# Optimization experiments

Measured on AMD Instinct MI355X. Metric: run time of the kernel, lower is better.

## Reference

```python
import jax, jax.numpy as jnp
import numpy as np

NUM_NODE = 64   # number of FPS nodes
NSAMPLE = 64    # ball-query / knn group size
RADIUS = 0.3    # first ball-query radius
K_INTERP = 3    # knn for upsample interpolation
BN_EPS = 1e-5


def sqdist(a, b):
    # a [B,S,3], b [B,N,3] -> squared distances [B,S,N]
    return (jnp.sum(a * a, -1)[:, :, None] + jnp.sum(b * b, -1)[:, None, :]
            - 2.0 * jnp.einsum('bsc,bnc->bsn', a, b))


def index_points(points, idx):
    # points [B,C,N] or [B,C,N,1]; idx [B,...] -> gathered [B,C,...]
    if points.ndim == 4:
        points = points[..., 0]
    return jax.vmap(lambda p, i: p[:, i])(points, idx)


def farthest_point_sample(xyz, npoint):
    # xyz [B,3,N] -> idx [B,npoint]; deterministic start at index 0
    B, C, N = xyz.shape

    def body(carry, _):
        dist, far = carry
        centroid = jnp.take_along_axis(xyz, far[:, None, None], axis=2)  # [B,3,1]
        d = jnp.sum((xyz - centroid) ** 2, axis=1)                       # [B,N]
        dist = jnp.minimum(dist, d)
        nxt = jnp.argmax(dist, axis=-1)
        return (dist, nxt), far

    init = (jnp.full((B, N), 1e10, xyz.dtype), jnp.zeros((B,), jnp.int32))
    _, idxs = jax.lax.scan(body, init, None, length=npoint)
    return idxs.T  # [B,npoint]


def query_ball_point(radius, nsample, xyz, new_xyz):
    # xyz [B,3,N], new_xyz [B,3,S] -> group idx [B,S,nsample]
    N = xyz.shape[2]
    sqr = sqdist(jnp.transpose(new_xyz, (0, 2, 1)), jnp.transpose(xyz, (0, 2, 1)))  # [B,S,N]
    if radius is not None:
        idx = jnp.broadcast_to(jnp.arange(N, dtype=jnp.int32), sqr.shape)
        idx = jnp.where(sqr > radius * radius, N, idx)
        idx = jnp.sort(idx, axis=-1)[:, :, :nsample]
        first = idx[:, :, :1]
        idx = jnp.where(idx == N, first, idx)  # pad misses with first hit
    else:
        idx = jnp.argsort(sqr, axis=-1)[:, :, :nsample].astype(jnp.int32)  # knn
    return idx


def _forward(input_fea, input_loc, pred_w, res_w, res_b, bn_gamma, bn_beta):
    # input_fea [B,C,N,1], input_loc [B,3,N]
    fidx = farthest_point_sample(input_loc, NUM_NODE)        # [B,S]
    fpoint_loc = index_points(input_loc, fidx)               # [B,3,S]
    fpoint_fea = index_points(input_fea, fidx)               # [B,C,S]

    gidx = query_ball_point(RADIUS, NSAMPLE, input_loc, fpoint_loc)  # [B,S,K]
    group_fea = index_points(input_fea, gidx) - fpoint_fea[..., None]  # [B,C,S,K]

    # pred_offset: 1x1 conv (no bias) + tanh
    seman = jnp.tanh(jnp.einsum('oc,bcsk->bosk', pred_w, group_fea))  # [B,3,S,K]

    group_loc = index_points(input_loc, gidx) - fpoint_loc[..., None]  # [B,3,S,K]
    node_offset = jnp.mean(seman * group_loc, axis=-1)       # [B,3,S]
    node_loc = fpoint_loc + node_offset                      # [B,3,S]

    gidx2 = query_ball_point(None, NSAMPLE, input_loc, node_loc)  # knn, [B,S,K]

    # residual branch: 1x1 conv + BatchNorm (training-mode batch stats) + ReLU
    res = jnp.einsum('oc,bcnk->bonk', res_w, input_fea) + res_b[None, :, None, None]
    mean = jnp.mean(res, axis=(0, 2, 3), keepdims=True)
    var = jnp.var(res, axis=(0, 2, 3), keepdims=True)
    res = (res - mean) * jax.lax.rsqrt(var + BN_EPS)
    res = jax.nn.relu(res * bn_gamma[None, :, None, None] + bn_beta[None, :, None, None])

    group_res = index_points(res, gidx2)                     # [B,F,S,K]
    node_fea = jnp.max(group_res, axis=-1, keepdims=True)    # [B,F,S,1]

    # upsample_inter: inverse-distance weighted 3-NN interpolation back to N points
    d = sqdist(jnp.transpose(input_loc, (0, 2, 1)), jnp.transpose(node_loc, (0, 2, 1)))  # [B,N,S]
    neg_d, kidx = jax.lax.top_k(-d, K_INTERP)                # k smallest dists
    dists = jnp.maximum(-neg_d, 1e-10)                       # [B,N,k]
    w = 1.0 / dists
    w = w / jnp.sum(w, axis=-1, keepdims=True)               # [B,N,k]
    interp = jnp.sum(index_points(node_fea, kidx) * w[:, None], axis=-1)  # [B,F,N]

    output_fea = jnp.concatenate([input_fea[..., 0], interp], axis=1)[..., None]  # [B,C+F,N,1]
    return output_fea, node_fea, node_offset


def setup_inputs() -> dict:
    key = jax.random.key(0)
    k1, k2, k3, k4, k5 = jax.random.split(key, 5)
    B, C, N = 32, 64, 8192
    FC = 64
    input_fea = jax.random.normal(k1, (B, C, N, 1), dtype=jnp.float32)
    input_loc = jax.random.uniform(k2, (B, 3, N), dtype=jnp.float32)
    pred_w = jax.random.normal(k3, (3, C), dtype=jnp.float32) * (1.0 / np.sqrt(C))
    res_w = jax.random.normal(k4, (FC, C), dtype=jnp.float32) * (1.0 / np.sqrt(C))
    res_b = jnp.zeros((FC,), dtype=jnp.float32)
    bn_gamma = jnp.ones((FC,), dtype=jnp.float32)
    bn_beta = jnp.zeros((FC,), dtype=jnp.float32)
    return {"input_fea": input_fea, "input_loc": input_loc, "pred_w": pred_w,
            "res_w": res_w, "res_b": res_b, "bn_gamma": bn_gamma, "bn_beta": bn_beta}


def reference(input_fea, input_loc, pred_w, res_w, res_b, bn_gamma, bn_beta):
    return _forward(input_fea, input_loc, pred_w, res_w, res_b, bn_gamma, bn_beta)
```

## Files before the change

kernel.cpp:

```cpp
#include <hip/hip_runtime.h>
#include <math.h>

#define BB 32
#define NN 8192
#define CC 64
#define SS 64
#define KK 64

#define WS_FIDX   0
#define WS_NLOC   270336
#define WS_GIDX2  276480
#define WS_PART   407552
#define WS_TOT    2537472
#define WS_SCALE  2541632
#define WS_SHIFT  2541696


__device__ __forceinline__ void fps_body(int b, const float* __restrict__ loc,
                                         int* __restrict__ fidx,
                                         float (*wrv)[8], int (*wri)[8],
                                         float (*wrx)[8], float (*wry)[8],
                                         float (*wrz)[8]) {
#pragma clang fp contract(off)
  __builtin_amdgcn_s_setprio(1);
  int t = threadIdx.x;
  const float* lb = loc + (size_t)b * 3 * NN;
  float px[16], py[16], pz[16], dist[16];
#pragma unroll
  for (int k = 0; k < 16; k++) {
    int p = t + 512 * k;
    px[k] = lb[p];
    py[k] = lb[NN + p];
    pz[k] = lb[2 * NN + p];
    dist[k] = 1e10f;
  }
  int lane = t & 63, w = t >> 6;
  int far = 0;
  float cx = lb[0], cy = lb[NN], cz = lb[2 * NN];
  for (int it = 0; it < 64; it++) {
    if (t == 0) fidx[b * 64 + it] = far;
    float bv = -1.0f; int bi = 0;
    float bx = 0.f, by = 0.f, bz = 0.f;
#pragma unroll
    for (int k = 0; k < 16; k++) {
      float dx = px[k] - cx, dy = py[k] - cy, dz = pz[k] - cz;
      float d = (dx * dx + dy * dy) + dz * dz;
      float dm = dist[k];
      dm = d < dm ? d : dm;
      dist[k] = dm;
      if (dm > bv) { bv = dm; bi = t + 512 * k; bx = px[k]; by = py[k]; bz = pz[k]; }
    }
    float v = bv; int vi = bi;
    float vx = bx, vy = by, vz = bz;
#pragma unroll
    for (int off = 1; off < 64; off <<= 1) {
      float v2 = __shfl_xor(v, off, 64);
      int   i2 = __shfl_xor(vi, off, 64);
      float x2 = __shfl_xor(vx, off, 64);
      float y2 = __shfl_xor(vy, off, 64);
      float z2 = __shfl_xor(vz, off, 64);
      if (v2 > v || (v2 == v && i2 < vi)) { v = v2; vi = i2; vx = x2; vy = y2; vz = z2; }
    }
    int par = it & 1;
    if (lane == 0) {
      wrv[par][w] = v; wri[par][w] = vi;
      wrx[par][w] = vx; wry[par][w] = vy; wrz[par][w] = vz;
    }
    __syncthreads();
    float gv = wrv[par][0]; int gi = wri[par][0];
    float gx = wrx[par][0], gy = wry[par][0], gz = wrz[par][0];
#pragma unroll
    for (int w2 = 1; w2 < 8; w2++) {
      float v2 = wrv[par][w2]; int i2 = wri[par][w2];
      if (v2 > gv || (v2 == gv && i2 < gi)) {
        gv = v2; gi = i2;
        gx = wrx[par][w2]; gy = wry[par][w2]; gz = wrz[par][w2];
      }
    }
    far = gi;
    cx = gx; cy = gy; cz = gz;
  }
}

__device__ __forceinline__ void transpose_body(int tb, const float* __restrict__ fea,
                                               float* __restrict__ feaT, float* tile) {
  int b = tb >> 7;
  int n0 = (tb & 127) * 64;
  int t = threadIdx.x;
  const float* fb = fea + (size_t)b * (CC * NN);
#pragma unroll
  for (int m = 0; m < 8; m++) {
    int idx = m * 512 + t;
    int c = idx >> 6, nl = idx & 63;
    tile[c * 65 + nl] = fb[(size_t)c * NN + n0 + nl];
  }
  __syncthreads();
  float* ob = feaT + ((size_t)b * NN + n0) * 64;
#pragma unroll
  for (int m = 0; m < 8; m++) {
    int idx = m * 512 + t;
    int nl = idx >> 6, c = idx & 63;
    ob[idx] = tile[c * 65 + nl];
  }
}

__device__ __forceinline__ void cov_body(int cb, const float* __restrict__ fea,
                                         float* __restrict__ part,
                                         float* Sf, float* red) {
  int t = threadIdx.x, w = t >> 6, lane = t & 63;
  int i = lane >> 3, j = lane & 7;
  float acc[8][8];
  float rs[8];
#pragma unroll
  for (int r = 0; r < 8; r++) {
    rs[r] = 0.f;
#pragma unroll
    for (int r2 = 0; r2 < 8; r2++) acc[r][r2] = 0.f;
  }
  for (int q = 0; q < 4; q++) {
    int chunk = cb * 4 + q;
    int p0 = chunk * 128;
    int b = p0 >> 13, n0 = p0 & 8191;
    __syncthreads();
    const float* fb = fea + (size_t)b * (CC * NN) + n0;
    for (int m = 0; m < 16; m++) {
      int idx = m * 512 + t;
      int c = idx >> 7, pt = idx & 127;
      Sf[c * 133 + pt] = fb[(size_t)c * NN + pt];
    }
    __syncthreads();
    if (w < 4) {
      for (int pt = w * 32; pt < w * 32 + 32; pt++) {
        float a[8], bv[8];
#pragma unroll
        for (int r = 0; r < 8; r++) {
          a[r] = Sf[(8 * i + r) * 133 + pt];
          bv[r] = Sf[(8 * j + r) * 133 + pt];
        }
#pragma unroll
        for (int r = 0; r < 8; r++) {
          rs[r] += a[r];
#pragma unroll
          for (int r2 = 0; r2 < 8; r2++) acc[r][r2] = fmaf(a[r], bv[r2], acc[r][r2]);
        }
      }
    }
  }
  for (int ww = 0; ww < 4; ww++) {
    if (w == ww) {
#pragma unroll
      for (int r = 0; r < 8; r++) {
#pragma unroll
        for (int r2 = 0; r2 < 8; r2++) {
          int idx = (8 * i + r) * 64 + 8 * j + r2;
          if (ww == 0) red[idx] = acc[r][r2]; else red[idx] += acc[r][r2];
        }
        if (j == 0) {
          int ridx = 4096 + 8 * i + r;
          if (ww == 0) red[ridx] = rs[r]; else red[ridx] += rs[r];
        }
      }
    }
    __syncthreads();
  }
  float* pb = part + (size_t)cb * 4160;
  for (int idx = t; idx < 4160; idx += 512) pb[idx] = red[idx];
}

__global__ __launch_bounds__(512, 1) void phase1_kernel(const float* __restrict__ fea,
                                                        const float* __restrict__ loc,
                                                        float* __restrict__ feaT,
                                                        int* __restrict__ fidx,
                                                        float* __restrict__ part) {
  __shared__ __align__(16) char smem[50688];
  __shared__ float wrv[2][8], wrx[2][8], wry[2][8], wrz[2][8];
  __shared__ int wri[2][8];
  int blk = blockIdx.x;
  if (blk < 32) {
    fps_body(blk, loc, fidx, wrv, wri, wrx, wry, wrz);
  } else if (blk < 4128) {
    transpose_body(blk - 32, fea, feaT, (float*)smem);
  } else {
    cov_body(blk - 4128, fea, part, (float*)smem, (float*)(smem + 34048));
  }
}

__global__ __launch_bounds__(256) void mega_kernel(const float* __restrict__ loc,
                                                   const float* __restrict__ feaT,
                                                   const float* __restrict__ pw,
                                                   const int* __restrict__ fidx,
                                                   const float* __restrict__ part,
                                                   float* __restrict__ tot,
                                                   int* __restrict__ gidx2,
                                                   float* __restrict__ out_noff,
                                                   float* __restrict__ nloc) {
#pragma clang fp contract(off)
  int blk = blockIdx.x;
  if (blk >= 2048) {
    int e = (blk - 2048) * 256 + threadIdx.x;
    if (e < 4160) {
      float sum = 0.f;
      for (int b2 = 0; b2 < 512; b2++) sum += part[(size_t)b2 * 4160 + e];
      tot[e] = sum;
    }
    return;
  }
  int bs = blk, b = bs >> 6, s = bs & 63, t = threadIdx.x;
  int lane = t & 63, w = t >> 6;
  __shared__ unsigned keys[NN];
  __shared__ unsigned hist[4096];
  __shared__ unsigned partl[256];
  __shared__ float sf[64];
  __shared__ float spw[192];
  __shared__ float sl[3];
  __shared__ float sA[3];
  __shared__ int gidxL[64];
  __shared__ int sP, sC0, nOut, nCand;
  const float* lb = loc + (size_t)b * 3 * NN;

  if (t < 192) spw[t] = pw[t];
  if (w == 0) {
    int g = fidx[bs];
    sf[lane] = feaT[((size_t)b * NN + g) * 64 + lane];
    if (lane < 3) sl[lane] = lb[(size_t)lane * NN + g];
  }
  __syncthreads();

  if (w == 0) {
    float ax = sl[0], ay = sl[1], az = sl[2];
    float A = (ax * ax + ay * ay) + az * az;
    int count = 0, firsth = -1;
    for (int ch = 0; ch < 128 && count < 64; ch++) {
      int p = ch * 64 + lane;
      float bx = lb[p], by = lb[NN + p], bz = lb[2 * NN + p];
      float Bn = (bx * bx + by * by) + bz * bz;
      float dot = fmaf(az, bz, fmaf(ay, by, ax * bx));
      float sqr = (A + Bn) - 2.0f * dot;
      bool hit = !(sqr > 0.09f);
      unsigned long long m = __ballot(hit);
      if (m) {
        if (firsth < 0) firsth = ch * 64 + (int)__ffsll(m) - 1;
        int pos = count + (int)__popcll(m & ((1ull << lane) - 1ull));
        if (hit && pos < 64) gidxL[pos] = p;
        count += (int)__popcll(m);
      }
    }
    if (count < 64 && lane >= count) gidxL[lane] = firsth;
  }
  __syncthreads();

  if (w == 0) {
    int g = gidxL[lane];
    const float* fT = feaT + ((size_t)b * NN + g) * 64;
    float a0 = 0.f, a1 = 0.f, a2 = 0.f;
#pragma unroll
    for (int c4 = 0; c4 < 16; c4++) {
      float4 f = *(const float4*)(fT + 4 * c4);
      int c = 4 * c4;
      float g0 = f.x - sf[c + 0];
      a0 = fmaf(spw[c + 0], g0, a0); a1 = fmaf(spw[64 + c + 0], g0, a1); a2 = fmaf(spw[128 + c + 0], g0, a2);
      float g1 = f.y - sf[c + 1];
      a0 = fmaf(spw[c + 1], g1, a0); a1 = fmaf(spw[64 + c + 1], g1, a1); a2 = fmaf(spw[128 + c + 1], g1, a2);
      float g2 = f.z - sf[c + 2];
      a0 = fmaf(spw[c + 2], g2, a0); a1 = fmaf(spw[64 + c + 2], g2, a1); a2 = fmaf(spw[128 + c + 2], g2, a2);
      float g3 = f.w - sf[c + 3];
      a0 = fmaf(spw[c + 3], g3, a0); a1 = fmaf(spw[64 + c + 3], g3, a1); a2 = fmaf(spw[128 + c + 3], g3, a2);
    }
    float c0 = tanhf(a0) * (lb[g] - sl[0]);
    float c1 = tanhf(a1) * (lb[NN + g] - sl[1]);
    float c2 = tanhf(a2) * (lb[2 * NN + g] - sl[2]);
#pragma unroll
    for (int off = 32; off; off >>= 1) {
      c0 += __shfl_xor(c0, off, 64);
      c1 += __shfl_xor(c1, off, 64);
      c2 += __shfl_xor(c2, off, 64);
    }
    if (lane == 0) {
      float m0 = c0 * (1.0f / 64), m1 = c1 * (1.0f / 64), m2 = c2 * (1.0f / 64);
      out_noff[b * 192 + s] = m0;
      out_noff[b * 192 + 64 + s] = m1;
      out_noff[b * 192 + 128 + s] = m2;
      float nx = sl[0] + m0, ny = sl[1] + m1, nz = sl[2] + m2;
      nloc[bs * 3 + 0] = nx;
      nloc[bs * 3 + 1] = ny;
      nloc[bs * 3 + 2] = nz;
      sA[0] = nx; sA[1] = ny; sA[2] = nz;
    }
  }
  __syncthreads();

  float ax = sA[0], ay = sA[1], az = sA[2];
  float A = (ax * ax + ay * ay) + az * az;
  for (int m = 0; m < 16; m++) hist[m * 256 + t] = 0u;
  if (t == 0) { nOut = 0; nCand = 0; }
  __syncthreads();
  unsigned mykey[32];
#pragma unroll
  for (int k = 0; k < 32; k++) {
    int p = t + 256 * k;
    float bx = lb[p], by = lb[NN + p], bz = lb[2 * NN + p];
    float Bn = (bx * bx + by * by) + bz * bz;
    float dot = fmaf(az, bz, fmaf(ay, by, ax * bx));
    float d = (A + Bn) - 2.0f * dot;
    unsigned kb = __float_as_uint(d);
    kb = (kb & 0x80000000u) ? ~kb : (kb | 0x80000000u);
    mykey[k] = kb;
    keys[p] = kb;
    atomicAdd(&hist[kb >> 20], 1u);
  }
  __syncthreads();
  unsigned ps = 0;
#pragma unroll
  for (int m = 0; m < 16; m++) ps += hist[t * 16 + m];
  partl[t] = ps;
  __syncthreads();
  if (t == 0) {
    int cum = 0, seg = 0;
    for (int t2 = 0; t2 < 256; t2++) {
      if (cum + (int)partl[t2] >= 64) { seg = t2; break; }
      cum += (int)partl[t2];
    }
    int P = seg * 16;
    for (;; P++) {
      if (cum + (int)hist[P] >= 64) break;
      cum += (int)hist[P];
    }
    sP = P; sC0 = cum;
  }
  __syncthreads();
  int P = sP, C0 = sC0;
  unsigned short* cand = (unsigned short*)hist;
  __syncthreads();
#pragma unroll
  for (int k = 0; k < 32; k++) {
    int bin = (int)(mykey[k] >> 20);
    if (bin < P) {
      int pos = atomicAdd(&nOut, 1);
      gidx2[bs * 64 + pos] = t + 256 * k;
    } else if (bin == P) {
      int c = atomicAdd(&nCand, 1);
      cand[c] = (unsigned short)(t + 256 * k);
    }
  }
  __syncthreads();
  if (t < 64) {
    int R = 64 - C0, nC = nCand;
    for (int r = 0; r < R; r++) {
      unsigned bk = 0xFFFFFFFFu; int bp = 0x7FFFFFFF, bj = -1;
      for (int j = lane; j < nC; j += 64) {
        int p = cand[j];
        if (p != 0xFFFF) {
          unsigned k2 = keys[p];
          if (k2 < bk || (k2 == bk && p < bp)) { bk = k2; bp = p; bj = j; }
        }
      }
#pragma unroll
      for (int off = 1; off < 64; off <<= 1) {
        unsigned k2 = __shfl_xor(bk, off, 64);
        int p2 = __shfl_xor(bp, off, 64);
        int j2 = __shfl_xor(bj, off, 64);
        if (k2 < bk || (k2 == bk && p2 < bp)) { bk = k2; bp = p2; bj = j2; }
      }
      if (lane == 0) {
        gidx2[bs * 64 + C0 + r] = bp;
        cand[bj] = 0xFFFF;
      }
      __threadfence_block();
    }
  }
}

__global__ __launch_bounds__(64) void bnstats_kernel(const float* __restrict__ tot,
                                                     const float* __restrict__ rw,
                                                     const float* __restrict__ rb,
                                                     const float* __restrict__ gam,
                                                     const float* __restrict__ bet,
                                                     float* __restrict__ bnsc,
                                                     float* __restrict__ bnsh) {
  int o = threadIdx.x;
  const float invM = 1.0f / 262144.0f;
  float mu = 0.f;
  for (int c = 0; c < 64; c++) mu += rw[o * 64 + c] * (tot[4096 + c] * invM);
  float exx = 0.f;
  for (int c = 0; c < 64; c++) {
    const float* row = tot + c * 64;
    float p = 0.f;
    for (int c2 = 0; c2 < 64; c2++) p += rw[o * 64 + c2] * row[c2];
    exx += rw[o * 64 + c] * p;
  }
  exx *= invM;
  float var = exx - mu * mu;
  float mean = mu + rb[o];
  float sc = gam[o] / sqrtf(var + 1e-5f);
  bnsc[o] = sc;
  bnsh[o] = bet[o] - mean * sc;
}

__global__ __launch_bounds__(256) void nodefea_kernel(const float* __restrict__ feaT,
                                                      const float* __restrict__ rw,
                                                      const int* __restrict__ gidx2,
                                                      const float* __restrict__ bnsc,
                                                      const float* __restrict__ bnsh,
                                                      float* __restrict__ out_nf) {
  __shared__ __align__(16) float Lf[4096];
  __shared__ float Lw[4096];
  __shared__ int Lg[64];
  __shared__ float red[256];
  int bs = blockIdx.x, b = bs >> 6, s = bs & 63, t = threadIdx.x;
  if (t < 64) Lg[t] = gidx2[bs * 64 + t];
  __syncthreads();
#pragma unroll
  for (int m = 0; m < 4; m++) {
    int idx4 = m * 256 + t;
    int k = idx4 >> 4, c4 = idx4 & 15;
    float4 f = *(const float4*)(feaT + ((size_t)b * NN + Lg[k]) * 64 + 4 * c4);
    *(float4*)&Lf[idx4 * 4] = f;
  }
  for (int m = 0; m < 16; m++) {
    int idx = m * 256 + t;
    Lw[idx] = rw[(idx & 63) * 64 + (idx >> 6)];
  }
  __syncthreads();
  int o = t & 63, wq = t >> 6;
  float wreg[64];
#pragma unroll
  for (int c = 0; c < 64; c++) wreg[c] = Lw[c * 64 + o];
  float sc = bnsc[o], sh = bnsh[o];
  float mx = -1e30f;
  for (int k = wq * 16; k < wq * 16 + 16; k++) {
    float raw = 0.f;
#pragma unroll
    for (int c4 = 0; c4 < 16; c4++) {
      float4 lf = *(const float4*)&Lf[k * 64 + c4 * 4];
      raw = fmaf(wreg[4 * c4 + 0], lf.x, raw);
      raw = fmaf(wreg[4 * c4 + 1], lf.y, raw);
      raw = fmaf(wreg[4 * c4 + 2], lf.z, raw);
      raw = fmaf(wreg[4 * c4 + 3], lf.w, raw);
    }
    float v = raw * sc + sh;
    v = v > 0.f ? v : 0.f;
    mx = v > mx ? v : mx;
  }
  red[wq * 64 + o] = mx;
  __syncthreads();
  if (t < 64) {
    float m0 = red[t], m1 = red[64 + t], m2 = red[128 + t], m3 = red[192 + t];
    float ma = m0 > m1 ? m0 : m1;
    float mb = m2 > m3 ? m2 : m3;
    float m = ma > mb ? ma : mb;
    out_nf[b * 4096 + t * 64 + s] = m;
  }
}

__global__ __launch_bounds__(256) void interp_kernel(const float* __restrict__ fea,
                                                     const float* __restrict__ loc,
                                                     const float* __restrict__ nloc,
                                                     const float* __restrict__ nf,
                                                     float* __restrict__ out) {
#pragma clang fp contract(off)
  int b = blockIdx.y;
  int t = threadIdx.x;
  int n = blockIdx.x * 256 + t;
  __shared__ float snl[192];
  __shared__ float sB[64];
  if (t < 192) snl[t] = nloc[b * 192 + t];
  __syncthreads();
  if (t < 64) {
    float x = snl[t * 3], y = snl[t * 3 + 1], z = snl[t * 3 + 2];
    sB[t] = (x * x + y * y) + z * z;
  }
  __syncthreads();
  const float* lb = loc + (size_t)b * 3 * NN;
  float px = lb[n], py = lb[NN + n], pz = lb[2 * NN + n];
  float A = (px * px + py * py) + pz * pz;
  float d0 = 1e30f, d1 = 1e30f, d2 = 1e30f;
  int i0 = 0, i1 = 0, i2 = 0;
  for (int s = 0; s < 64; s++) {
    float dot = fmaf(pz, snl[s * 3 + 2], fmaf(py, snl[s * 3 + 1], px * snl[s * 3]));
    float d = (A + sB[s]) - 2.0f * dot;
    if (d < d0) { d2 = d1; i2 = i1; d1 = d0; i1 = i0; d0 = d; i0 = s; }
    else if (d < d1) { d2 = d1; i2 = i1; d1 = d; i1 = s; }
    else if (d < d2) { d2 = d; i2 = s; }
  }
  d0 = d0 > 1e-10f ? d0 : 1e-10f;
  d1 = d1 > 1e-10f ? d1 : 1e-10f;
  d2 = d2 > 1e-10f ? d2 : 1e-10f;
  float r0 = 1.0f / d0, r1 = 1.0f / d1, r2 = 1.0f / d2;
  float rsum = (r0 + r1) + r2;
  float w0 = r0 / rsum, w1 = r1 / rsum, w2 = r2 / rsum;
  const float* nfb = nf + b * 4096;
  const float* fb = fea + (size_t)b * (CC * NN);
  float* ob = out + (size_t)b * (128 * NN);
  for (int o = 0; o < 64; o++) {
    ob[(size_t)o * NN + n] = fb[(size_t)o * NN + n];
    float ip = (nfb[o * 64 + i0] * w0 + nfb[o * 64 + i1] * w1) + nfb[o * 64 + i2] * w2;
    ob[(size_t)(64 + o) * NN + n] = ip;
  }
}

extern "C" void kernel_launch(void* const* d_in, const int* in_sizes, int n_in,
                              void* d_out, int out_size, void* d_ws, size_t ws_size,
                              hipStream_t stream) {
  (void)in_sizes; (void)n_in; (void)out_size; (void)ws_size;
  const float* fea = (const float*)d_in[0];
  const float* loc = (const float*)d_in[1];
  const float* pw  = (const float*)d_in[2];
  const float* rw  = (const float*)d_in[3];
  const float* rb  = (const float*)d_in[4];
  const float* gam = (const float*)d_in[5];
  const float* bet = (const float*)d_in[6];
  float* out = (float*)d_out;
  float* ws = (float*)d_ws;

  int*   fidx  = (int*)(ws + WS_FIDX);
  float* nlocp = ws + WS_NLOC;
  int*   gidx2 = (int*)(ws + WS_GIDX2);
  float* part  = ws + WS_PART;
  float* tot   = ws + WS_TOT;
  float* bnsc  = ws + WS_SCALE;
  float* bnsh  = ws + WS_SHIFT;

  float* feaT     = out;
  float* out_nf   = out + 33554432;
  float* out_noff = out + 33685504;

  phase1_kernel<<<dim3(4640), dim3(512), 0, stream>>>(fea, loc, feaT, fidx, part);
  mega_kernel<<<dim3(2065), dim3(256), 0, stream>>>(loc, feaT, pw, fidx, part, tot,
                                                    gidx2, out_noff, nlocp);
  bnstats_kernel<<<dim3(1), dim3(64), 0, stream>>>(tot, rw, rb, gam, bet, bnsc, bnsh);
  nodefea_kernel<<<dim3(2048), dim3(256), 0, stream>>>(feaT, rw, gidx2, bnsc, bnsh, out_nf);
  interp_kernel<<<dim3(32, 32), dim3(256), 0, stream>>>(fea, loc, nlocp, out_nf, out);
}
```

Measured before the change: 604.9 us.

## Parallelize ball-query scan, register-resident kNN tie selection, stage node features in LDS

The radius ball-query scan now runs across all four wavefronts, each writing hit ballot masks to shared memory, instead of only wave 0 walking all chunks serially. The kNN boundary-bin selection drops the 8192-entry shared keys array and the candidate list, and does iterative min-selection directly over register keys across the whole block, with a barrier per selected element. The interpolation kernel stages the per-batch node feature table in LDS so the three-neighbor gathers hit shared memory instead of global. The tradeoffs are the loss of the ball query's early exit once 64 hits are found, and extra block-wide synchronisation in the selection loop.

```diff
diff --git a/kernel.cpp b/kernel.cpp
--- a/kernel.cpp
+++ b/kernel.cpp
@@ -207,7 +207,7 @@
   }
   int bs = blk, b = bs >> 6, s = bs & 63, t = threadIdx.x;
   int lane = t & 63, w = t >> 6;
-  __shared__ unsigned keys[NN];
+  __shared__ unsigned long long masks[128];
   __shared__ unsigned hist[4096];
   __shared__ unsigned partl[256];
   __shared__ float sf[64];
@@ -215,7 +215,11 @@
   __shared__ float sl[3];
   __shared__ float sA[3];
   __shared__ int gidxL[64];
-  __shared__ int sP, sC0, nOut, nCand;
+  __shared__ unsigned wrk[4];
+  __shared__ int wrp[4];
+  __shared__ unsigned selk;
+  __shared__ int selp;
+  __shared__ int sP, sC0, nOut;
   const float* lb = loc + (size_t)b * 3 * NN;
 
   if (t < 192) spw[t] = pw[t];
@@ -226,11 +230,11 @@
   }
   __syncthreads();
 
-  if (w == 0) {
+  {
     float ax = sl[0], ay = sl[1], az = sl[2];
     float A = (ax * ax + ay * ay) + az * az;
-    int count = 0, firsth = -1;
-    for (int ch = 0; ch < 128 && count < 64; ch++) {
+    for (int cc = 0; cc < 32; cc++) {
+      int ch = w * 32 + cc;
       int p = ch * 64 + lane;
       float bx = lb[p], by = lb[NN + p], bz = lb[2 * NN + p];
       float Bn = (bx * bx + by * by) + bz * bz;
@@ -238,10 +242,20 @@
       float sqr = (A + Bn) - 2.0f * dot;
       bool hit = !(sqr > 0.09f);
       unsigned long long m = __ballot(hit);
+      if (lane == 0) masks[ch] = m;
+    }
+  }
+  __syncthreads();
+
+  if (w == 0) {
+    int count = 0, firsth = -1;
+    for (int ch = 0; ch < 128 && count < 64; ch++) {
+      unsigned long long m = masks[ch];
       if (m) {
         if (firsth < 0) firsth = ch * 64 + (int)__ffsll(m) - 1;
+        bool hit = (m >> lane) & 1ull;
         int pos = count + (int)__popcll(m & ((1ull << lane) - 1ull));
-        if (hit && pos < 64) gidxL[pos] = p;
+        if (hit && pos < 64) gidxL[pos] = ch * 64 + lane;
         count += (int)__popcll(m);
       }
     }
@@ -292,7 +306,7 @@
   float ax = sA[0], ay = sA[1], az = sA[2];
   float A = (ax * ax + ay * ay) + az * az;
   for (int m = 0; m < 16; m++) hist[m * 256 + t] = 0u;
-  if (t == 0) { nOut = 0; nCand = 0; }
+  if (t == 0) nOut = 0;
   __syncthreads();
   unsigned mykey[32];
 #pragma unroll
@@ -305,7 +319,6 @@
     unsigned kb = __float_as_uint(d);
     kb = (kb & 0x80000000u) ? ~kb : (kb | 0x80000000u);
     mykey[k] = kb;
-    keys[p] = kb;
     atomicAdd(&hist[kb >> 20], 1u);
   }
   __syncthreads();
@@ -329,44 +342,46 @@
   }
   __syncthreads();
   int P = sP, C0 = sC0;
-  unsigned short* cand = (unsigned short*)hist;
-  __syncthreads();
 #pragma unroll
   for (int k = 0; k < 32; k++) {
-    int bin = (int)(mykey[k] >> 20);
-    if (bin < P) {
+    if ((int)(mykey[k] >> 20) < P) {
       int pos = atomicAdd(&nOut, 1);
       gidx2[bs * 64 + pos] = t + 256 * k;
-    } else if (bin == P) {
-      int c = atomicAdd(&nCand, 1);
-      cand[c] = (unsigned short)(t + 256 * k);
-    }
-  }
-  __syncthreads();
-  if (t < 64) {
-    int R = 64 - C0, nC = nCand;
-    for (int r = 0; r < R; r++) {
-      unsigned bk = 0xFFFFFFFFu; int bp = 0x7FFFFFFF, bj = -1;
-      for (int j = lane; j < nC; j += 64) {
-        int p = cand[j];
-        if (p != 0xFFFF) {
-          unsigned k2 = keys[p];
-          if (k2 < bk || (k2 == bk && p < bp)) { bk = k2; bp = p; bj = j; }
-        }
+    }
+  }
+  int R = 64 - C0;
+  unsigned lastk = 0u; int lastp = -1;
+  for (int r = 0; r < R; r++) {
+    unsigned bk = 0xFFFFFFFFu; int bp = 0x7FFFFFFF;
+#pragma unroll
+    for (int k = 0; k < 32; k++) {
+      unsigned kk = mykey[k];
+      if ((int)(kk >> 20) == P) {
+        int p = t + 256 * k;
+        bool gt = (kk > lastk) || (kk == lastk && p > lastp);
+        if (gt && (kk < bk || (kk == bk && p < bp))) { bk = kk; bp = p; }
       }
-#pragma unroll
-      for (int off = 1; off < 64; off <<= 1) {
-        unsigned k2 = __shfl_xor(bk, off, 64);
-        int p2 = __shfl_xor(bp, off, 64);
-        int j2 = __shfl_xor(bj, off, 64);
-        if (k2 < bk || (k2 == bk && p2 < bp)) { bk = k2; bp = p2; bj = j2; }
+    }
+#pragma unroll
+    for (int off = 1; off < 64; off <<= 1) {
+      unsigned k2 = __shfl_xor(bk, off, 64);
+      int p2 = __shfl_xor(bp, off, 64);
+      if (k2 < bk || (k2 == bk && p2 < bp)) { bk = k2; bp = p2; }
+    }
+    if (lane == 0) { wrk[w] = bk; wrp[w] = bp; }
+    __syncthreads();
+    if (t == 0) {
+      unsigned fk = wrk[0]; int fp = wrp[0];
+#pragma unroll
+      for (int w2 = 1; w2 < 4; w2++) {
+        unsigned k2 = wrk[w2]; int p2 = wrp[w2];
+        if (k2 < fk || (k2 == fk && p2 < fp)) { fk = k2; fp = p2; }
       }
-      if (lane == 0) {
-        gidx2[bs * 64 + C0 + r] = bp;
-        cand[bj] = 0xFFFF;
-      }
-      __threadfence_block();
-    }
+      gidx2[bs * 64 + C0 + r] = fp;
+      selk = fk; selp = fp;
+    }
+    __syncthreads();
+    lastk = selk; lastp = selp;
   }
 }
 
@@ -463,7 +478,13 @@
   int n = blockIdx.x * 256 + t;
   __shared__ float snl[192];
   __shared__ float sB[64];
+  __shared__ float snf[4096];
   if (t < 192) snl[t] = nloc[b * 192 + t];
+  {
+    const float* nfb = nf + b * 4096;
+#pragma unroll
+    for (int m = 0; m < 16; m++) snf[m * 256 + t] = nfb[m * 256 + t];
+  }
   __syncthreads();
   if (t < 64) {
     float x = snl[t * 3], y = snl[t * 3 + 1], z = snl[t * 3 + 2];
@@ -488,12 +509,11 @@
   float r0 = 1.0f / d0, r1 = 1.0f / d1, r2 = 1.0f / d2;
   float rsum = (r0 + r1) + r2;
   float w0 = r0 / rsum, w1 = r1 / rsum, w2 = r2 / rsum;
-  const float* nfb = nf + b * 4096;
   const float* fb = fea + (size_t)b * (CC * NN);
   float* ob = out + (size_t)b * (128 * NN);
   for (int o = 0; o < 64; o++) {
     ob[(size_t)o * NN + n] = fb[(size_t)o * NN + n];
-    float ip = (nfb[o * 64 + i0] * w0 + nfb[o * 64 + i1] * w1) + nfb[o * 64 + i2] * w2;
+    float ip = (snf[o * 64 + i0] * w0 + snf[o * 64 + i1] * w1) + snf[o * 64 + i2] * w2;
     ob[(size_t)(64 + o) * NN + n] = ip;
   }
 }
```

New measurement: 648.1 us. +7.1%, slower.
